# Optimization experiments

Hardware: AMD Instinct MI355X
Metric: run time of the kernel (lower is better)

## Reference

```python
import jax, jax.numpy as jnp
import numpy as np

HEADS = 4
NBLK = 4
UPS = 4
EPS = 1e-5


def conv3x3(x, w, b):
    # x: NCHW, w: OIHW (3x3, stride 1, pad 1 -> SAME)
    y = jax.lax.conv_general_dilated(x, w, (1, 1), 'SAME',
                                     dimension_numbers=('NCHW', 'OIHW', 'NCHW'))
    return y + b[None, :, None, None]


def layer_norm(x, g, b):
    mu = jnp.mean(x, axis=-1, keepdims=True)
    var = jnp.var(x, axis=-1, keepdims=True)
    return (x - mu) * jax.lax.rsqrt(var + EPS) * g + b


def attention(x, wq, bq, wp, bp):
    # NOTE: the torch module's reshape flattens all windows into one sequence,
    # so this is mathematically global attention over all H*W tokens.
    B, H, W, C = x.shape
    L = H * W
    hd = C // HEADS
    t = x.reshape(B, L, C)
    qkv = (t @ wq + bq).reshape(B, L, 3, HEADS, hd).transpose(2, 0, 3, 1, 4)
    q, k, v = qkv[0], qkv[1], qkv[2]                      # (B, nh, L, hd)
    attn = jax.nn.softmax(jnp.einsum('bnld,bnmd->bnlm', q, k) * (hd ** -0.5), axis=-1)
    o = jnp.einsum('bnlm,bnmd->bnld', attn, v)            # (B, nh, L, hd)
    o = o.transpose(0, 2, 1, 3).reshape(B, L, C)
    return (o @ wp + bp).reshape(B, H, W, C)


def swin_block(x, g1, b1, wq, bq, wp, bp, g2, b2, w1, bf1, w2, bf2):
    shortcut = x
    h = jnp.transpose(x, (0, 2, 3, 1))                    # NHWC
    h = layer_norm(h, g1, b1)
    h = attention(h, wq, bq, wp, bp) + h
    h = layer_norm(h, g2, b2)
    h = (jax.nn.gelu(h @ w1 + bf1, approximate=False) @ w2 + bf2) + h
    return shortcut + jnp.transpose(h, (0, 3, 1, 2))


def pixel_shuffle(x, r):
    B, C, H, W = x.shape
    c = C // (r * r)
    x = x.reshape(B, c, r, r, H, W).transpose(0, 1, 4, 2, 5, 3)
    return x.reshape(B, c, H * r, W * r)


def setup_inputs() -> dict:
    key = jax.random.key(0)
    ks = jax.random.split(key, 16)
    d = 48

    def rn(k, shape, s=0.02):
        return jax.random.normal(k, shape, jnp.float32) * s

    return {
        'x': jax.random.normal(ks[0], (2, 3, 64, 64), jnp.float32),
        'conv_first_w': rn(ks[1], (d, 3, 3, 3)),
        'conv_first_b': jnp.zeros((d,), jnp.float32),
        'norm1_g': jnp.ones((NBLK, d), jnp.float32),
        'norm1_b': jnp.zeros((NBLK, d), jnp.float32),
        'qkv_w': rn(ks[2], (NBLK, d, 3 * d)),
        'qkv_b': jnp.zeros((NBLK, 3 * d), jnp.float32),
        'proj_w': rn(ks[3], (NBLK, d, d)),
        'proj_b': jnp.zeros((NBLK, d), jnp.float32),
        'norm2_g': jnp.ones((NBLK, d), jnp.float32),
        'norm2_b': jnp.zeros((NBLK, d), jnp.float32),
        'fc1_w': rn(ks[4], (NBLK, d, 2 * d)),
        'fc1_b': jnp.zeros((NBLK, 2 * d), jnp.float32),
        'fc2_w': rn(ks[5], (NBLK, 2 * d, d)),
        'fc2_b': jnp.zeros((NBLK, d), jnp.float32),
        'up_w': rn(ks[6], (d * UPS * UPS, d, 3, 3)),
        'up_b': jnp.zeros((d * UPS * UPS,), jnp.float32),
        'last_w': rn(ks[7], (3, d, 3, 3)),
        'last_b': jnp.zeros((3,), jnp.float32),
    }


def reference(x, conv_first_w, conv_first_b, norm1_g, norm1_b, qkv_w, qkv_b,
              proj_w, proj_b, norm2_g, norm2_b, fc1_w, fc1_b, fc2_w, fc2_b,
              up_w, up_b, last_w, last_b):
    h = conv3x3(x, conv_first_w, conv_first_b)
    for i in range(NBLK):
        h = swin_block(h, norm1_g[i], norm1_b[i], qkv_w[i], qkv_b[i],
                       proj_w[i], proj_b[i], norm2_g[i], norm2_b[i],
                       fc1_w[i], fc1_b[i], fc2_w[i], fc2_b[i])
    h = conv3x3(h, up_w, up_b)
    h = pixel_shuffle(h, UPS)
    return conv3x3(h, last_w, last_b)
```

## Files before the change

### kernel.cpp

```cpp
#include <hip/hip_runtime.h>
#include <hip/hip_bf16.h>
#include <math.h>

#define BB 2
#define D 48
#define HH 64
#define WW 64
#define LL 4096
#define NHEADS 4
#define HD 12
#define NBLK 4
#define CUP 768
#define H2 256
#define W2 256

#define NSPLIT 4
#define OPART_STRIDE 393216

typedef __attribute__((ext_vector_type(8))) short short8v;
typedef __attribute__((ext_vector_type(4))) float f32x4;
typedef unsigned long long u64;

__device__ __forceinline__ short f2bf(float f) {
    __hip_bfloat16 h = __float2bfloat16(f);
    union { __hip_bfloat16 b; short s; } u; u.b = h; return u.s;
}
__device__ __forceinline__ float bf2f(short s) {
    union { float f; unsigned u; } x;
    x.u = ((unsigned)(unsigned short)s) << 16;
    return x.f;
}
__device__ __forceinline__ float exp2_raw(float x) {
    float r; asm("v_exp_f32 %0, %1" : "=v"(r) : "v"(x)); return r;
}

__global__ void conv3x3_kernel(const float* __restrict__ in, const float* __restrict__ w,
                               const float* __restrict__ bias, float* __restrict__ out,
                               int Cin, int Cout) {
    int idx = blockIdx.x * blockDim.x + threadIdx.x;
    int total = BB * Cout * HH * WW;
    if (idx >= total) return;
    int x = idx % WW;
    int y = (idx / WW) % HH;
    int co = (idx / (WW * HH)) % Cout;
    int b = idx / (WW * HH * Cout);
    float s = bias[co];
    for (int ci = 0; ci < Cin; ci++) {
        const float* ip = in + ((size_t)(b * Cin + ci) * HH) * WW;
        const float* wp = w + (size_t)(co * Cin + ci) * 9;
        #pragma unroll
        for (int ky = 0; ky < 3; ky++) {
            int iy = y + ky - 1;
            if (iy < 0 || iy >= HH) continue;
            #pragma unroll
            for (int kx = 0; kx < 3; kx++) {
                int ix = x + kx - 1;
                if (ix < 0 || ix >= WW) continue;
                s += ip[iy * WW + ix] * wp[ky * 3 + kx];
            }
        }
    }
    out[idx] = s;
}

__global__ __launch_bounds__(256) void pack_h_kernel(const float* __restrict__ h,
                                                     short* __restrict__ hbfp) {
    int idx = blockIdx.x * 256 + threadIdx.x;
    const int TOT = 2 * 66 * 66 * 48;
    if (idx >= TOT + 64) return;
    if (idx >= TOT) { hbfp[idx] = 0; return; }
    int ci = idx % 48;
    int p = idx / 48;
    int xx = p % 66;
    int q = p / 66;
    int yy = q % 66;
    int b = q / 66;
    short v = 0;
    if (yy >= 1 && yy <= 64 && xx >= 1 && xx <= 64)
        v = f2bf(h[((size_t)(b * 48 + ci) << 12) + (yy - 1) * 64 + (xx - 1)]);
    hbfp[idx] = v;
}

__global__ __launch_bounds__(256) void pack_w_kernel(const float* __restrict__ w,
                                                     short* __restrict__ Wp) {
    int idx = blockIdx.x * 256 + threadIdx.x;
    if (idx >= 48 * 14 * 512) return;
    int j = idx & 7;
    int g = (idx >> 3) & 3;
    int col = (idx >> 5) & 15;
    int s = (idx >> 9) % 14;
    int n16 = idx / (14 * 512);
    int k = 32 * s + 8 * g + j;
    short v = 0;
    if (k < 432) {
        int tap = k / 48, ci = k - tap * 48;
        int co = n16 * 16 + col;
        v = f2bf(w[((size_t)co * 48 + ci) * 9 + tap]);
    }
    Wp[idx] = v;
}

__global__ __launch_bounds__(256) void conv_up_mfma_kernel(const short* __restrict__ hbfp,
                                                           const short* __restrict__ Wp,
                                                           const float* __restrict__ bias,
                                                           short* __restrict__ U) {
    int tid = threadIdx.x;
    int wave = tid >> 6, lane = tid & 63;
    int t = blockIdx.x * 4 + wave;
    int mt = t / 48;
    int n16 = t - mt * 48;
    int b = mt >> 8;
    int rem = mt & 255;
    int y = rem >> 2;
    int xt = rem & 3;
    int col = lane & 15;
    int g = lane >> 4;
    int x = xt * 16 + col;

    const short* Bp = Wp + (size_t)n16 * (14 * 512) + col * 32 + g * 8;
    const short* zb = hbfp + 2 * 66 * 66 * 48;

    f32x4 acc = {0.f, 0.f, 0.f, 0.f};
    #pragma unroll
    for (int s = 0; s < 14; s++) {
        int gg = 4 * s + g;
        int tap = (gg * 171) >> 10;
        int cig = gg - tap * 6;
        int dy = (tap * 11) >> 5;
        int dx = tap - dy * 3;
        const short* ap = hbfp + ((size_t)((b * 66 + y + dy) * 66 + (x + dx)) * 48 + cig * 8);
        ap = (gg < 54) ? ap : zb;
        short8v av = *(const short8v*)ap;
        short8v bv = *(const short8v*)(Bp + s * 512);
        acc = __builtin_amdgcn_mfma_f32_16x16x32_bf16(av, bv, acc, 0, 0, 0);
    }

    int co = n16 * 16 + col;
    float bval = bias[co];
    int ic = co >> 4, dyq = (co >> 2) & 3, dxq = co & 3;
    short* Ur = U + ((size_t)(b * 48 + ic) * 256 + 4 * y + dyq) * 256 + dxq;
    #pragma unroll
    for (int j = 0; j < 4; j++) {
        int r = 4 * g + j;
        Ur[4 * (xt * 16 + r)] = f2bf(acc[j] + bval);
    }
}

__global__ void zero16_kernel(u64* __restrict__ p, int n) {
    int i = blockIdx.x * 256 + threadIdx.x;
    if (i >= n) return;
    u64 fill = 0ull;
    int rel = 8 * i - 2097152;
    if (rel >= 0 && rel < 524288 && (((rel >> 5) & 15) == 12))
        fill = 0x3F803F803F803F80ull;
    p[2 * i] = fill;
    p[2 * i + 1] = fill;
}

__global__ __launch_bounds__(256) void fused_ln1_qkv_kernel(
    const float* __restrict__ hsrc, const float* __restrict__ g1, const float* __restrict__ b1,
    const float* __restrict__ w, const float* __restrict__ bias,
    float* __restrict__ ln1, short* __restrict__ Qbf, short* __restrict__ Kbf,
    short* __restrict__ Vr) {
    __shared__ float hs[48 * 17];
    __shared__ float lnr[16 * 49];
    __shared__ float wl[48 * 144];
    int blk = blockIdx.x;
    int b = blk >> 8;
    int pos0 = (blk & 255) * 16;
    int tid = threadIdx.x;

    for (int i = tid; i < 48 * 144; i += 256) wl[i] = w[i];
    for (int i = tid; i < 48 * 16; i += 256) {
        int ch = i >> 4, p = i & 15;
        hs[ch * 17 + p] = hsrc[((size_t)b * 48 + ch) * 4096 + pos0 + p];
    }
    __syncthreads();

    int tok = tid >> 4, oct = tid & 15;
    int pos = pos0 + tok;
    float v[3];
    float s = 0.f, s2 = 0.f;
    #pragma unroll
    for (int j = 0; j < 3; j++) {
        float x = hs[(oct * 3 + j) * 17 + tok];
        v[j] = x; s += x; s2 += x * x;
    }
    #pragma unroll
    for (int msk = 1; msk < 16; msk <<= 1) {
        s += __shfl_xor(s, msk, 64);
        s2 += __shfl_xor(s2, msk, 64);
    }
    float mu = s * (1.f / 48.f);
    float var = s2 * (1.f / 48.f) - mu * mu;
    float rs = rsqrtf(var + 1e-5f);
    float* go = ln1 + ((size_t)b * 4096 + pos) * 48 + oct * 3;
    #pragma unroll
    for (int j = 0; j < 3; j++) {
        int c = oct * 3 + j;
        float y = (v[j] - mu) * rs * g1[c] + b1[c];
        lnr[tok * 49 + c] = y;
        go[j] = y;
    }
    __syncthreads();

    int c0 = oct * 9;
    float acc[9];
    #pragma unroll
    for (int j = 0; j < 9; j++) acc[j] = bias[c0 + j];
    #pragma unroll 4
    for (int k = 0; k < 48; k++) {
        float a = lnr[tok * 49 + k];
        const float* wr = wl + k * 144 + c0;
        #pragma unroll
        for (int j = 0; j < 9; j++) acc[j] += a * wr[j];
    }

    const float scale = 0.41647023f;
    int sstep = pos >> 5, r = pos & 31;
    int g2 = (r < 16) ? (r >> 2) : ((r - 16) >> 2);
    int j2 = (r < 16) ? (r & 3) : 4 + ((r - 16) & 3);
    #pragma unroll
    for (int j = 0; j < 9; j++) {
        int c = c0 + j;
        int which = (c >= 96) ? 2 : (c >= 48 ? 1 : 0);
        int rem = c - which * 48;
        int hh = rem / 12;
        int dd = rem - hh * 12;
        int bh = b * 4 + hh;
        if (which == 0)
            Qbf[((size_t)bh * 4096 + pos) * 32 + dd] = f2bf(acc[j] * scale);
        else if (which == 1)
            Kbf[((size_t)bh * 4096 + pos) * 32 + dd] = f2bf(acc[j]);
        else
            Vr[((size_t)bh * 128 + sstep) * 512 + dd * 32 + g2 * 8 + j2] = f2bf(acc[j]);
    }
}

__global__ __launch_bounds__(256) void fused_mlp_kernel(
    const float* __restrict__ opart, const float* __restrict__ ssump,
    const float* __restrict__ pwg, const float* __restrict__ pb,
    const float* __restrict__ ln1, const float* __restrict__ g2v, const float* __restrict__ b2v,
    const float* __restrict__ f1w, const float* __restrict__ f1b,
    const float* __restrict__ f2w, const float* __restrict__ f2b,
    float* __restrict__ hbuf) {
    __shared__ float sm[14640];
    float* wp  = sm;
    float* w1  = sm + 2304;
    float* w2  = sm + 6912;
    float* arf = sm + 11520;
    float* lnr = sm + 12304;
    float* m1v = sm + 13088;

    int blk = blockIdx.x;
    int b = blk >> 8;
    int pos0 = (blk & 255) * 16;
    int tid = threadIdx.x;

    for (int i = tid; i < 2304; i += 256) wp[i] = pwg[i];
    for (int i = tid; i < 4608; i += 256) w1[i] = f1w[i];
    for (int i = tid; i < 4608; i += 256) w2[i] = f2w[i];
    for (int i = tid; i < 768; i += 256) {
        int t = i / 48, c = i - (i / 48) * 48;
        int hh = c / 12;
        size_t base = ((size_t)b * 4096 + pos0) * 48 + i;
        float stot = 0.f, s = 0.f;
        #pragma unroll
        for (int sp = 0; sp < NSPLIT; sp++) {
            stot += ssump[((size_t)sp * 8 + b * 4 + hh) * 4096 + pos0 + t];
            s += opart[base + (size_t)sp * OPART_STRIDE];
        }
        arf[t * 49 + c] = s / stot;
    }
    __syncthreads();

    int tok = tid >> 4, oct = tid & 15;
    size_t gtok = (size_t)b * 4096 + pos0 + tok;
    int c0 = oct * 3;
    float acc[3];
    #pragma unroll
    for (int j = 0; j < 3; j++) acc[j] = pb[c0 + j];
    #pragma unroll 4
    for (int k = 0; k < 48; k++) {
        float a = arf[tok * 49 + k];
        const float* wr = wp + k * 48 + c0;
        #pragma unroll
        for (int j = 0; j < 3; j++) acc[j] += a * wr[j];
    }
    const float* rp = ln1 + gtok * 48 + c0;
    float x[3]; float s = 0.f, s2 = 0.f;
    #pragma unroll
    for (int j = 0; j < 3; j++) {
        float t = acc[j] + rp[j];
        x[j] = t; s += t; s2 += t * t;
    }
    #pragma unroll
    for (int msk = 1; msk < 16; msk <<= 1) {
        s += __shfl_xor(s, msk, 64);
        s2 += __shfl_xor(s2, msk, 64);
    }
    float mu = s * (1.f / 48.f), var = s2 * (1.f / 48.f) - mu * mu;
    float rs = rsqrtf(var + 1e-5f);
    #pragma unroll
    for (int j = 0; j < 3; j++) {
        int c = c0 + j;
        lnr[tok * 49 + c] = (x[j] - mu) * rs * g2v[c] + b2v[c];
    }
    __syncthreads();

    int d0 = oct * 6;
    float a2[6];
    #pragma unroll
    for (int j = 0; j < 6; j++) a2[j] = f1b[d0 + j];
    #pragma unroll 4
    for (int k = 0; k < 48; k++) {
        float a = lnr[tok * 49 + k];
        const float* wr = w1 + k * 96 + d0;
        #pragma unroll
        for (int j = 0; j < 6; j++) a2[j] += a * wr[j];
    }
    #pragma unroll
    for (int j = 0; j < 6; j++) {
        float g = a2[j];
        m1v[tok * 97 + d0 + j] = 0.5f * g * (1.f + erff(g * 0.70710678118654752f));
    }
    __syncthreads();

    float f2acc[3];
    #pragma unroll
    for (int j = 0; j < 3; j++) f2acc[j] = f2b[c0 + j];
    #pragma unroll 4
    for (int k = 0; k < 96; k++) {
        float a = m1v[tok * 97 + k];
        const float* wr = w2 + k * 48 + c0;
        #pragma unroll
        for (int j = 0; j < 3; j++) f2acc[j] += a * wr[j];
    }
    __syncthreads();
    #pragma unroll
    for (int j = 0; j < 3; j++)
        arf[tok * 49 + c0 + j] = f2acc[j] + lnr[tok * 49 + c0 + j];
    __syncthreads();

    for (int i = tid; i < 768; i += 256) {
        int c = i >> 4, t = i & 15;
        hbuf[(((size_t)(b * 48 + c)) << 12) + pos0 + t] += arf[t * 49 + c];
    }
}

#define LOADCH(P, c) { \
    _Pragma("unroll") \
    for (int s_ = 0; s_ < 4; s_++) { \
        const short* kp_ = Kb + ((size_t)((c) * 128 + s_ * 32 + col)) * 32 + g * 8; \
        P##k0[s_] = *(const short8v*)(kp_); \
        P##k1[s_] = *(const short8v*)(kp_ + 512); \
        P##v[s_]  = *(const short8v*)(Vrb + ((c) * 4 + s_) * 512 + vbase); \
    } }

#define STEP2(kc0, kc1, vv) { \
    f32x4 z_ = {0.f, 0.f, 0.f, 0.f}; \
    f32x4 sa1 = __builtin_amdgcn_mfma_f32_16x16x32_bf16(kc0, qb0, z_, 0, 0, 0); \
    f32x4 sa2 = __builtin_amdgcn_mfma_f32_16x16x32_bf16(kc1, qb0, z_, 0, 0, 0); \
    f32x4 sb1 = __builtin_amdgcn_mfma_f32_16x16x32_bf16(kc0, qb1, z_, 0, 0, 0); \
    f32x4 sb2 = __builtin_amdgcn_mfma_f32_16x16x32_bf16(kc1, qb1, z_, 0, 0, 0); \
    float a0 = exp2_raw(sa1[0]), a1 = exp2_raw(sa1[1]); \
    float a2 = exp2_raw(sa1[2]), a3 = exp2_raw(sa1[3]); \
    float a4 = exp2_raw(sa2[0]), a5 = exp2_raw(sa2[1]); \
    float a6 = exp2_raw(sa2[2]), a7 = exp2_raw(sa2[3]); \
    float e0 = exp2_raw(sb1[0]), e1 = exp2_raw(sb1[1]); \
    float e2 = exp2_raw(sb1[2]), e3 = exp2_raw(sb1[3]); \
    float e4 = exp2_raw(sb2[0]), e5 = exp2_raw(sb2[1]); \
    float e6 = exp2_raw(sb2[2]), e7 = exp2_raw(sb2[3]); \
    union { short8v sv; unsigned u[4]; } pa_, pe_; \
    asm("v_cvt_pk_bf16_f32 %0, %1, %2" : "=v"(pa_.u[0]) : "v"(a0), "v"(a1)); \
    asm("v_cvt_pk_bf16_f32 %0, %1, %2" : "=v"(pa_.u[1]) : "v"(a2), "v"(a3)); \
    asm("v_cvt_pk_bf16_f32 %0, %1, %2" : "=v"(pa_.u[2]) : "v"(a4), "v"(a5)); \
    asm("v_cvt_pk_bf16_f32 %0, %1, %2" : "=v"(pa_.u[3]) : "v"(a6), "v"(a7)); \
    asm("v_cvt_pk_bf16_f32 %0, %1, %2" : "=v"(pe_.u[0]) : "v"(e0), "v"(e1)); \
    asm("v_cvt_pk_bf16_f32 %0, %1, %2" : "=v"(pe_.u[1]) : "v"(e2), "v"(e3)); \
    asm("v_cvt_pk_bf16_f32 %0, %1, %2" : "=v"(pe_.u[2]) : "v"(e4), "v"(e5)); \
    asm("v_cvt_pk_bf16_f32 %0, %1, %2" : "=v"(pe_.u[3]) : "v"(e6), "v"(e7)); \
    o0 = __builtin_amdgcn_mfma_f32_16x16x32_bf16(vv, pa_.sv, o0, 0, 0, 0); \
    o1 = __builtin_amdgcn_mfma_f32_16x16x32_bf16(vv, pe_.sv, o1, 0, 0, 0); }

#define COMPUTECH2(P) { \
    STEP2(P##k0[0], P##k1[0], P##v[0]); \
    STEP2(P##k0[1], P##k1[1], P##v[1]); \
    STEP2(P##k0[2], P##k1[2], P##v[2]); \
    STEP2(P##k0[3], P##k1[3], P##v[3]); }

__global__ __launch_bounds__(256) void attn_mfma_kernel(const short* __restrict__ Qbf,
                                                        const short* __restrict__ Kbf,
                                                        const short* __restrict__ Vr,
                                                        float* __restrict__ opart,
                                                        float* __restrict__ ssump) {
    int bid = blockIdx.x;
    int bh = bid & 7;
    int qblk = (bid >> 3) & 31;
    int split = bid >> 8;
    int h = bh & 3, b = bh >> 2;
    int tid = threadIdx.x;
    int wave = tid >> 6;
    int lane = tid & 63;
    int q0 = qblk * 128 + wave * 32;
    int col = lane & 15;
    int g = lane >> 4;

    const short* Kb  = Kbf + (size_t)bh * LL * 32 + (size_t)split * 1024 * 32;
    const short* Vrb = Vr + (size_t)bh * 65536 + (size_t)split * 32 * 512;
    int vbase = col * 32 + g * 8;

    short8v qb0 = *(const short8v*)(Qbf + ((size_t)bh * LL + q0 + col) * 32 + g * 8);
    short8v qb1 = *(const short8v*)(Qbf + ((size_t)bh * LL + q0 + 16 + col) * 32 + g * 8);

    f32x4 o0 = {0.f, 0.f, 0.f, 0.f};
    f32x4 o1 = {0.f, 0.f, 0.f, 0.f};

    short8v a_k0[4], a_k1[4], a_v[4];
    short8v b_k0[4], b_k1[4], b_v[4];

    LOADCH(a_, 0);
    for (int c = 0; c < 8; c += 2) {
        LOADCH(b_, c + 1);
        COMPUTECH2(a_);
        if (c + 2 < 8) LOADCH(a_, c + 2);
        COMPUTECH2(b_);
    }

    float ssa = __shfl(o0[0], 48 + col, 64);
    float ssb = __shfl(o1[0], 48 + col, 64);

    float* op = opart + (size_t)split * OPART_STRIDE
              + ((size_t)b * 4096 + q0 + col) * 48 + h * HD;
    #pragma unroll
    for (int j = 0; j < 4; j++) {
        int d = 4 * g + j;
        if (d < HD) {
            op[d] = o0[j];
            op[16 * 48 + d] = o1[j];
        }
    }
    if (lane < 16) {
        float* sp = ssump + ((size_t)split * 8 + bh) * 4096 + q0 + col;
        sp[0] = ssa;
        sp[16] = ssb;
    }
}

#define LW2 36
__global__ __launch_bounds__(128) void lastconv_kernel(const short* __restrict__ U,
                                                       const float* __restrict__ w,
                                                       const float* __restrict__ bias,
                                                       float* __restrict__ out) {
    int blk = blockIdx.x;
    int xt = blk & 7;
    int yt = (blk >> 3) & 63;
    int b = blk >> 9;
    int tid = threadIdx.x;
    int xx = tid & 31;
    int yy = tid >> 5;
    int y0 = yt * 4;
    int x0t = xt * 32;
    int y = y0 + yy;
    int x = x0t + xx;

    __shared__ float wl[3 * 48 * 9];
    __shared__ float tile[2][6 * LW2];
    for (int i = tid; i < 3 * 48 * 9; i += 128) wl[i] = w[i];

    const short* Ub = U + (size_t)b * 48 * 65536;

    int soff[2]; int doff[2]; bool sval[2]; bool swr[2];
    #pragma unroll
    for (int kk = 0; kk < 2; kk++) {
        int i = tid + kk * 128;
        int r = i / 34, c = i - r * 34;
        int gy = y0 - 1 + r, gx = x0t - 1 + c;
        bool inb_ok = (i < 204);
        bool ok = inb_ok && (gy >= 0 && gy < 256 && gx >= 0 && gx < 256);
        swr[kk] = inb_ok;
        sval[kk] = ok;
        doff[kk] = inb_ok ? r * LW2 + c : 0;
        soff[kk] = ok ? gy * 256 + gx : 0;
    }

    {
        float* tb = tile[0];
        #pragma unroll
        for (int kk = 0; kk < 2; kk++)
            if (swr[kk]) tb[doff[kk]] = sval[kk] ? bf2f(Ub[soff[kk]]) : 0.f;
    }

    float acc[3];
    #pragma unroll
    for (int oc = 0; oc < 3; oc++) acc[oc] = bias[oc];
    __syncthreads();

    for (int ci = 0; ci < 48; ci++) {
        float rr[2];
        if (ci + 1 < 48) {
            const short* ip = Ub + (size_t)(ci + 1) * 65536;
            #pragma unroll
            for (int kk = 0; kk < 2; kk++)
                rr[kk] = sval[kk] ? bf2f(ip[soff[kk]]) : 0.f;
        }
        const float* tp = tile[ci & 1];
        float row[3][3];
        #pragma unroll
        for (int ky = 0; ky < 3; ky++) {
            const float* rp = tp + (yy + ky) * LW2 + xx;
            #pragma unroll
            for (int dx = 0; dx < 3; dx++) row[ky][dx] = rp[dx];
        }
        #pragma unroll
        for (int oc = 0; oc < 3; oc++) {
            const float* wp = wl + (oc * 48 + ci) * 9;
            acc[oc] += wp[0] * row[0][0] + wp[1] * row[0][1] + wp[2] * row[0][2]
                     + wp[3] * row[1][0] + wp[4] * row[1][1] + wp[5] * row[1][2]
                     + wp[6] * row[2][0] + wp[7] * row[2][1] + wp[8] * row[2][2];
        }
        if (ci + 1 < 48) {
            float* tb = tile[(ci + 1) & 1];
            #pragma unroll
            for (int kk = 0; kk < 2; kk++)
                if (swr[kk]) tb[doff[kk]] = rr[kk];
        }
        __syncthreads();
    }
    #pragma unroll
    for (int oc = 0; oc < 3; oc++)
        out[(((size_t)(b * 3 + oc) * 256) + y) * 256 + x] = acc[oc];
}

static inline int gs(int n) { return (n + 255) / 256; }

extern "C" void kernel_launch(void* const* d_in, const int* in_sizes, int n_in,
                              void* d_out, int out_size, void* d_ws, size_t ws_size,
                              hipStream_t stream) {
    const float* x    = (const float*)d_in[0];
    const float* cf_w = (const float*)d_in[1];
    const float* cf_b = (const float*)d_in[2];
    const float* n1g  = (const float*)d_in[3];
    const float* n1b  = (const float*)d_in[4];
    const float* qkvw = (const float*)d_in[5];
    const float* qkvb = (const float*)d_in[6];
    const float* pw   = (const float*)d_in[7];
    const float* pb   = (const float*)d_in[8];
    const float* n2g  = (const float*)d_in[9];
    const float* n2b  = (const float*)d_in[10];
    const float* f1w  = (const float*)d_in[11];
    const float* f1b  = (const float*)d_in[12];
    const float* f2w  = (const float*)d_in[13];
    const float* f2b  = (const float*)d_in[14];
    const float* upw  = (const float*)d_in[15];
    const float* upb  = (const float*)d_in[16];
    const float* lw   = (const float*)d_in[17];
    const float* lb   = (const float*)d_in[18];

    float* ws = (float*)d_ws;
    const int S_h = BB * D * LL;
    float* A_h   = ws;
    float* pool  = ws + S_h;
    float* A_ln1 = pool;

    short* U_bf = (short*)pool;
    float* o_part = pool + 1572864;
    short* hbfp = (short*)(pool + 3145728);
    short* Wp   = (short*)(pool + 3145728 + 209120);
    short* Qbf  = (short*)(pool + 3538944);
    short* Kbf  = Qbf + BB * NHEADS * LL * 32;
    short* Vr   = Kbf + BB * NHEADS * LL * 32;
    float* ssum_part = pool + 5898240;

    conv3x3_kernel<<<gs(S_h), 256, 0, stream>>>(x, cf_w, cf_b, A_h, 3, D);

    zero16_kernel<<<1536, 256, 0, stream>>>((u64*)Qbf, 393216);
    pack_w_kernel<<<1344, 256, 0, stream>>>(upw, Wp);

    for (int i = 0; i < NBLK; i++) {
        fused_ln1_qkv_kernel<<<512, 256, 0, stream>>>(
            A_h, n1g + i * D, n1b + i * D,
            qkvw + (size_t)i * D * 3 * D, qkvb + i * 3 * D,
            A_ln1, Qbf, Kbf, Vr);
        attn_mfma_kernel<<<8 * 32 * NSPLIT, 256, 0, stream>>>(Qbf, Kbf, Vr, o_part, ssum_part);
        fused_mlp_kernel<<<512, 256, 0, stream>>>(
            o_part, ssum_part, pw + (size_t)i * D * D, pb + i * D,
            A_ln1, n2g + i * D, n2b + i * D,
            f1w + (size_t)i * D * 2 * D, f1b + i * 2 * D,
            f2w + (size_t)i * 2 * D * D, f2b + i * D,
            A_h);
    }

    pack_h_kernel<<<1634, 256, 0, stream>>>(A_h, hbfp);
    conv_up_mfma_kernel<<<6144, 256, 0, stream>>>(hbfp, Wp, upb, U_bf);

    lastconv_kernel<<<1024, 128, 0, stream>>>(U_bf, lw, lb, (float*)d_out);
}
```

Measured before the change: 322.6 us.

## Switch final conv to bf16 MFMA with channels-last upsampled layout

The final 3x3 convolution (48->3 channels at 256x256) moves from a scalar FMA kernel with shared-memory tiles to an MFMA implicit-GEMM kernel. The output columns are padded to 16, and only 3 of them are kept. To support this, the upsample conv now writes its pixel-shuffled output in NHWC (channels-last) order, so each lane loads 8 contiguous channels per tap. A new pack kernel prepares bf16 weights, and workspace buffers are relocated. The cost is wasted MFMA columns and more scattered, strided writes in the upsample conv epilogue.

Result: faster. 310.0 us (-3.9%).

```diff
diff --git a/kernel.cpp b/kernel.cpp
--- a/kernel.cpp
+++ b/kernel.cpp
@@ -100,6 +100,23 @@
     Wp[idx] = v;
 }
 
+__global__ __launch_bounds__(256) void pack_lw_kernel(const float* __restrict__ w,
+                                                      short* __restrict__ Wp2) {
+    int idx = blockIdx.x * 256 + threadIdx.x;
+    if (idx >= 14 * 512) return;
+    int j = idx & 7;
+    int g = (idx >> 3) & 3;
+    int col = (idx >> 5) & 15;
+    int s = idx >> 9;
+    int k = 32 * s + 8 * g + j;
+    short v = 0;
+    if (k < 432 && col < 3) {
+        int tap = k / 48, ci = k - tap * 48;
+        v = f2bf(w[((size_t)col * 48 + ci) * 9 + tap]);
+    }
+    Wp2[idx] = v;
+}
+
 __global__ __launch_bounds__(256) void conv_up_mfma_kernel(const short* __restrict__ hbfp,
                                                            const short* __restrict__ Wp,
                                                            const float* __restrict__ bias,
@@ -138,11 +155,13 @@
     int co = n16 * 16 + col;
     float bval = bias[co];
     int ic = co >> 4, dyq = (co >> 2) & 3, dxq = co & 3;
-    short* Ur = U + ((size_t)(b * 48 + ic) * 256 + 4 * y + dyq) * 256 + dxq;
+    int y2 = 4 * y + dyq;
+    short* Ur = U + ((size_t)(b * 256 + y2) * 256) * 48 + ic;
     #pragma unroll
     for (int j = 0; j < 4; j++) {
         int r = 4 * g + j;
-        Ur[4 * (xt * 16 + r)] = f2bf(acc[j] + bval);
+        int x2 = 4 * (xt * 16 + r) + dxq;
+        Ur[(size_t)x2 * 48] = f2bf(acc[j] + bval);
     }
 }
 
@@ -447,89 +466,48 @@
     }
 }
 
-#define LW2 36
-__global__ __launch_bounds__(128) void lastconv_kernel(const short* __restrict__ U,
-                                                       const float* __restrict__ w,
-                                                       const float* __restrict__ bias,
-                                                       float* __restrict__ out) {
-    int blk = blockIdx.x;
-    int xt = blk & 7;
-    int yt = (blk >> 3) & 63;
-    int b = blk >> 9;
+__global__ __launch_bounds__(256) void lastconv_mfma_kernel(const short* __restrict__ U,
+                                                            const short* __restrict__ Wp2,
+                                                            const short* __restrict__ zb,
+                                                            const float* __restrict__ bias,
+                                                            float* __restrict__ out) {
     int tid = threadIdx.x;
-    int xx = tid & 31;
-    int yy = tid >> 5;
-    int y0 = yt * 4;
-    int x0t = xt * 32;
-    int y = y0 + yy;
-    int x = x0t + xx;
-
-    __shared__ float wl[3 * 48 * 9];
-    __shared__ float tile[2][6 * LW2];
-    for (int i = tid; i < 3 * 48 * 9; i += 128) wl[i] = w[i];
-
-    const short* Ub = U + (size_t)b * 48 * 65536;
-
-    int soff[2]; int doff[2]; bool sval[2]; bool swr[2];
-    #pragma unroll
-    for (int kk = 0; kk < 2; kk++) {
-        int i = tid + kk * 128;
-        int r = i / 34, c = i - r * 34;
-        int gy = y0 - 1 + r, gx = x0t - 1 + c;
-        bool inb_ok = (i < 204);
-        bool ok = inb_ok && (gy >= 0 && gy < 256 && gx >= 0 && gx < 256);
-        swr[kk] = inb_ok;
-        sval[kk] = ok;
-        doff[kk] = inb_ok ? r * LW2 + c : 0;
-        soff[kk] = ok ? gy * 256 + gx : 0;
-    }
-
-    {
-        float* tb = tile[0];
-        #pragma unroll
-        for (int kk = 0; kk < 2; kk++)
-            if (swr[kk]) tb[doff[kk]] = sval[kk] ? bf2f(Ub[soff[kk]]) : 0.f;
-    }
-
-    float acc[3];
-    #pragma unroll
-    for (int oc = 0; oc < 3; oc++) acc[oc] = bias[oc];
-    __syncthreads();
-
-    for (int ci = 0; ci < 48; ci++) {
-        float rr[2];
-        if (ci + 1 < 48) {
-            const short* ip = Ub + (size_t)(ci + 1) * 65536;
-            #pragma unroll
-            for (int kk = 0; kk < 2; kk++)
-                rr[kk] = sval[kk] ? bf2f(ip[soff[kk]]) : 0.f;
-        }
-        const float* tp = tile[ci & 1];
-        float row[3][3];
-        #pragma unroll
-        for (int ky = 0; ky < 3; ky++) {
-            const float* rp = tp + (yy + ky) * LW2 + xx;
-            #pragma unroll
-            for (int dx = 0; dx < 3; dx++) row[ky][dx] = rp[dx];
-        }
-        #pragma unroll
-        for (int oc = 0; oc < 3; oc++) {
-            const float* wp = wl + (oc * 48 + ci) * 9;
-            acc[oc] += wp[0] * row[0][0] + wp[1] * row[0][1] + wp[2] * row[0][2]
-                     + wp[3] * row[1][0] + wp[4] * row[1][1] + wp[5] * row[1][2]
-                     + wp[6] * row[2][0] + wp[7] * row[2][1] + wp[8] * row[2][2];
-        }
-        if (ci + 1 < 48) {
-            float* tb = tile[(ci + 1) & 1];
-            #pragma unroll
-            for (int kk = 0; kk < 2; kk++)
-                if (swr[kk]) tb[doff[kk]] = rr[kk];
-        }
-        __syncthreads();
-    }
-    #pragma unroll
-    for (int oc = 0; oc < 3; oc++)
-        out[(((size_t)(b * 3 + oc) * 256) + y) * 256 + x] = acc[oc];
+    int wave = tid >> 6, lane = tid & 63;
+    int t = blockIdx.x * 4 + wave;
+    int xt = t & 15;
+    int yy = (t >> 4) & 255;
+    int b = t >> 12;
+    int col = lane & 15, g = lane >> 4;
+    int x = xt * 16 + col;
+
+    const short* Ub = U + (size_t)b * 65536 * 48;
+    const short* Bp = Wp2 + col * 32 + g * 8;
+
+    f32x4 acc = {0.f, 0.f, 0.f, 0.f};
+    #pragma unroll
+    for (int s = 0; s < 14; s++) {
+        int gg = 4 * s + g;
+        int tap = (gg * 171) >> 10;
+        int cig = gg - tap * 6;
+        int dy3 = (tap * 11) >> 5;
+        int dy = dy3 - 1;
+        int dx = tap - dy3 * 3 - 1;
+        int yq = yy + dy, xq = x + dx;
+        bool ok = (gg < 54) && (yq >= 0) && (yq < 256) && (xq >= 0) && (xq < 256);
+        const short* ap = Ub + (ptrdiff_t)(yq * 256 + xq) * 48 + cig * 8;
+        ap = ok ? ap : zb;
+        short8v av = *(const short8v*)ap;
+        short8v bv = *(const short8v*)(Bp + s * 512);
+        acc = __builtin_amdgcn_mfma_f32_16x16x32_bf16(av, bv, acc, 0, 0, 0);
+    }
+
+    if (col < 3) {
+        float bval = bias[col];
+        float* op = out + ((size_t)(b * 3 + col) * 256 + yy) * 256 + xt * 16 + 4 * g;
+        #pragma unroll
+        for (int j = 0; j < 4; j++)
+            op[j] = acc[j] + bval;
+    }
 }
 
 static inline int gs(int n) { return (n + 255) / 256; }
@@ -565,17 +543,19 @@
 
     short* U_bf = (short*)pool;
     float* o_part = pool + 1572864;
-    short* hbfp = (short*)(pool + 3145728);
-    short* Wp   = (short*)(pool + 3145728 + 209120);
     short* Qbf  = (short*)(pool + 3538944);
     short* Kbf  = Qbf + BB * NHEADS * LL * 32;
     short* Vr   = Kbf + BB * NHEADS * LL * 32;
+    short* hbfp = (short*)(pool + 4849664);
+    short* Wp   = (short*)(pool + 5058784);
+    short* Wp2  = (short*)(pool + 5230816);
     float* ssum_part = pool + 5898240;
 
     conv3x3_kernel<<<gs(S_h), 256, 0, stream>>>(x, cf_w, cf_b, A_h, 3, D);
 
     zero16_kernel<<<1536, 256, 0, stream>>>((u64*)Qbf, 393216);
     pack_w_kernel<<<1344, 256, 0, stream>>>(upw, Wp);
+    pack_lw_kernel<<<28, 256, 0, stream>>>(lw, Wp2);
 
     for (int i = 0; i < NBLK; i++) {
         fused_ln1_qkv_kernel<<<512, 256, 0, stream>>>(
@@ -594,5 +574,6 @@
     pack_h_kernel<<<1634, 256, 0, stream>>>(A_h, hbfp);
     conv_up_mfma_kernel<<<6144, 256, 0, stream>>>(hbfp, Wp, upb, U_bf);
 
-    lastconv_kernel<<<1024, 128, 0, stream>>>(U_bf, lw, lb, (float*)d_out);
-}
+    lastconv_mfma_kernel<<<2048, 256, 0, stream>>>(
+        U_bf, Wp2, hbfp + 2 * 66 * 66 * 48, lb, (float*)d_out);
+}
```
